# Kernel tuning notes

Hardware: AMD Instinct MI355X
Metric: run time of the kernel (lower is better)

Reference implementation:

```python
import jax, jax.numpy as jnp
import numpy as np

DIM = 512
N_HEADS = 8
N_LAYERS = 2
N_BLOCKS = 9 * N_LAYERS
B = 8
L_LEN = V_LEN = A_LEN = 512
L_DIM, V_DIM, A_DIM = 768, 640, 205
N_CLASSES = 9


def setup_inputs() -> dict:
    key = jax.random.key(0)
    ks = jax.random.split(key, 16)
    s = 0.02
    return {
        'l': jax.random.normal(ks[0], (B, L_LEN, L_DIM), jnp.float32),
        'v': jax.random.normal(ks[1], (B, V_LEN, V_DIM), jnp.float32),
        'a': jax.random.normal(ks[2], (B, A_LEN, A_DIM), jnp.float32),
        'l_mask': jnp.ones((B, L_LEN), jnp.float32),
        'v_mask': jnp.ones((B, V_LEN), jnp.float32),
        'a_mask': jnp.ones((B, A_LEN), jnp.float32),
        'wl': jax.random.normal(ks[3], (L_DIM, DIM), jnp.float32) * s,
        'wv': jax.random.normal(ks[4], (V_DIM, DIM), jnp.float32) * s,
        'wa': jax.random.normal(ks[5], (A_DIM, DIM), jnp.float32) * s,
        'n1_g': jnp.ones((DIM,), jnp.float32),
        'n1_b': jnp.zeros((DIM,), jnp.float32),
        'proj_w': jax.random.normal(ks[6], (N_BLOCKS, DIM, DIM), jnp.float32) * s,
        'minus_w': jax.random.normal(ks[7], (N_BLOCKS, 2 * DIM, DIM), jnp.float32) * s,
        'n2_g': jnp.ones((N_BLOCKS, DIM), jnp.float32),
        'n2_b': jnp.zeros((N_BLOCKS, DIM), jnp.float32),
        'c': jnp.full((N_BLOCKS,), 0.1, jnp.float32),
        'clf_w': jax.random.normal(ks[8], (6 * N_LAYERS * DIM, N_CLASSES), jnp.float32) * s,
    }


def _ln(x, g, b, eps=1e-5):
    mu = jnp.mean(x, axis=-1, keepdims=True)
    var = jnp.mean((x - mu) ** 2, axis=-1, keepdims=True)
    return (x - mu) * jax.lax.rsqrt(var + eps) * g + b


def reference(l, v, a, l_mask, v_mask, a_mask, wl, wv, wa, n1_g, n1_b,
              proj_w, minus_w, n2_g, n2_b, c, clf_w):
    hd = DIM // N_HEADS
    inv_sqrt = 1.0 / np.sqrt(hd).astype(np.float32)

    def block(i, q_in, kv, mask, scores_prev):
        Bq, Lq, D = q_in.shape
        qh = q_in.reshape(Bq, Lq, N_HEADS, hd)
        kh = kv.reshape(Bq, kv.shape[1], N_HEADS, hd)  # k and v are the same raw tensor
        scores = jnp.einsum('bqhd,bkhd->bhqk', qh, kh) * inv_sqrt
        if scores_prev is not None:
            scores = scores + c[i] * scores_prev
        scores = scores - 1e8 * (1.0 - mask[:, None, None, :])
        att = jax.nn.softmax(scores, axis=-1)
        ctx = jnp.einsum('bhqk,bkhd->bqhd', att, kh).reshape(Bq, Lq, D)
        x = ctx @ proj_w[i]  # proj, no bias; dropout is identity (eval)
        out = _ln(jnp.concatenate([q_in, x], axis=-1) @ minus_w[i], n2_g[i], n2_b[i])
        return out, scores

    def stream(q0, kv, mask, off, outs):
        q, s = q0, None
        for j in range(N_LAYERS):
            q, s = block(off * N_LAYERS + j, q, kv, mask, s)
            outs.append(q)

    # Unify_Dimension
    lu = _ln(l @ wl, n1_g, n1_b)
    vu = _ln(v @ wv, n1_g, n1_b)
    au = _ln(a @ wa, n1_g, n1_b)

    l_list, v_list, a_list = [], [], []
    stream(lu, lu, l_mask, 0, l_list)
    stream(lu, vu, v_mask, 1, l_list)
    stream(lu, au, a_mask, 2, l_list)
    stream(vu, vu, v_mask, 3, v_list)
    stream(vu, lu, l_mask, 4, v_list)
    stream(vu, au, a_mask, 5, v_list)
    stream(au, au, a_mask, 6, a_list)
    stream(au, lu, l_mask, 7, a_list)
    stream(au, vu, v_mask, 8, a_list)

    lc = jnp.concatenate(l_list, axis=2)  # [B, l_len, 3*n_layers*dim]
    vc = jnp.concatenate(v_list, axis=2)
    ac = jnp.concatenate(a_list, axis=2)
    x = jnp.concatenate([lc, ac, vc], axis=1)  # note order: l, a, v (as in source)
    feats = jnp.concatenate([jnp.mean(x, axis=1), jnp.max(x, axis=1)], axis=1)
    return feats @ clf_w
```

## Files before the change

### kernel.cpp

```cpp
#include <hip/hip_runtime.h>
#include <cstdint>
#include <cstddef>

#define DEV __device__ __forceinline__

typedef __attribute__((ext_vector_type(8))) short short8;
typedef __attribute__((ext_vector_type(4))) float floatx4;
typedef unsigned short u16;
typedef unsigned int u32;

union Frag { short8 s8; uint4 u4; uint2 u2[2]; u16 us[8]; };

DEV float b2f(u16 u) { union { float f; u32 i; } v; v.i = ((u32)u) << 16; return v.f; }
DEV u16 f2b(float f) {
  union { float f; u32 i; } v; v.f = f; u32 x = v.i;
  return (u16)((x + 0x7fffu + ((x >> 16) & 1u)) >> 16);
}
DEV floatx4 mfma16(short8 a, short8 b, floatx4 c) {
  return __builtin_amdgcn_mfma_f32_16x16x32_bf16(a, b, c, 0, 0, 0);
}
DEV void gl_lds16(const u16* g, u16* l) {
  __builtin_amdgcn_global_load_lds(
      (const __attribute__((address_space(1))) void*)g,
      (__attribute__((address_space(3))) void*)l, 16, 0, 0);
}

__global__ void det_kernel(const u32* __restrict__ mask, int* __restrict__ flag)
{
  if (threadIdx.x == 0 && blockIdx.x == 0)
    *flag = (mask[0] == 0x3F803F80u) ? 0 : 1;
}

struct ConvArgs {
  const void* src[17];
  u16* dst[17];
  int n[17];
  int bstart[17];
};

__global__ __launch_bounds__(256, 4)
void convert_all_kernel(ConvArgs a, const int* __restrict__ flag)
{
  const int bid = blockIdx.x;
  int seg = 0;
  #pragma unroll
  for (int i = 1; i < 17; i++) if (bid >= a.bstart[i]) seg = i;
  const int n = a.n[seg];
  const int base = (bid - a.bstart[seg]) * 1024 + threadIdx.x * 4;
  if (base >= n) return;
  const int f32mode = *flag;
  if (base + 4 <= n) {
    union { uint2 v; u16 u[4]; } o;
    if (f32mode) {
      const float* s = (const float*)a.src[seg] + base;
      float4 f = *(const float4*)s;
      o.u[0] = f2b(f.x); o.u[1] = f2b(f.y); o.u[2] = f2b(f.z); o.u[3] = f2b(f.w);
    } else {
      o.v = *(const uint2*)((const u16*)a.src[seg] + base);
    }
    *(uint2*)(a.dst[seg] + base) = o.v;
  } else {
    for (int k = base; k < n; k++) {
      if (f32mode) a.dst[seg][k] = f2b(((const float*)a.src[seg])[k]);
      else         a.dst[seg][k] = ((const u16*)a.src[seg])[k];
    }
  }
}

__global__ __launch_bounds__(256, 2)
void transpose_kernel(const u16* __restrict__ S, u16* __restrict__ D,
                      int R, int dstStride, int srcZ, int dstZ)
{
  __shared__ u16 tile[64 * 72];
  const u16* src = S + (size_t)blockIdx.z * srcZ;
  u16* dst = D + (size_t)blockIdx.z * dstZ;
  const int r0 = blockIdx.x * 64, c0 = blockIdx.y * 64;
  const int t = threadIdx.x;
  const int row = t >> 2, cc = (t & 3) * 16;
  if (r0 + 64 <= R) {
    uint4 v0 = *(const uint4*)(src + (size_t)(r0 + row) * 512 + c0 + cc);
    uint4 v1 = *(const uint4*)(src + (size_t)(r0 + row) * 512 + c0 + cc + 8);
    *(uint4*)&tile[row * 72 + cc] = v0;
    *(uint4*)&tile[row * 72 + cc + 8] = v1;
  } else {
    bool ok = (r0 + row) < R;
    for (int j = 0; j < 16; j++)
      tile[row * 72 + cc + j] = ok ? src[(size_t)(r0 + row) * 512 + c0 + cc + j] : (u16)0;
  }
  __syncthreads();
  const int cl = t >> 2, rc = (t & 3) * 16;
  if (r0 + 64 <= dstStride) {
    union { uint4 v[2]; u16 u[16]; } o;
    #pragma unroll
    for (int j = 0; j < 16; j++) o.u[j] = tile[(rc + j) * 72 + cl];
    u16* gd = dst + (size_t)(c0 + cl) * dstStride + r0 + rc;
    *(uint4*)gd = o.v[0];
    *(uint4*)(gd + 8) = o.v[1];
  } else {
    for (int j = 0; j < 16; j++) {
      int rr = r0 + rc + j;
      if (rr < dstStride) dst[(size_t)(c0 + cl) * dstStride + rr] = tile[(rc + j) * 72 + cl];
    }
  }
}

__global__ __launch_bounds__(256, 4)
void gemm_kernel(const u16* __restrict__ A1, int lda1, int az1,
                 const u16* __restrict__ A2, int lda2, int az2,
                 const u16* __restrict__ B1, int ldb1, int bz1,
                 const u16* __restrict__ B2, int ldb2, int bz2,
                 u16* __restrict__ O, int oz,
                 int Ktot, int Ksplit, int KAvalid, int flags)
{
  __shared__ u16 gbuf[18432];
  u16* As = gbuf;
  u16* Bs = gbuf + 4096;

  const int z = blockIdx.z;
  const int m0 = blockIdx.x * 128, n0 = blockIdx.y * 128;
  const int t = threadIdx.x, w = t >> 6, l = t & 63, l15 = l & 15, quad = l >> 4;
  const int zA = (flags & 4) ? (z / 3) : z;
  const u16* A1p = A1 + (size_t)zA * az1;
  const u16* A2p = A2 ? (A2 + (size_t)z * az2) : nullptr;
  const u16* B1p = B1 + (size_t)z * bz1;
  const u16* B2p = B2 ? (B2 + (size_t)z * bz2) : nullptr;
  u16* Op = O + (size_t)z * oz;

  const int c0r = t >> 2;
  const int c0k = t & 3;
  u16* AsW = As + (size_t)t * 8;
  u16* BsW = Bs + (size_t)t * 8;

  floatx4 acc[4][4];
  #pragma unroll
  for (int i = 0; i < 4; i++)
    #pragma unroll
    for (int j = 0; j < 4; j++) {
      acc[i][j][0] = 0.f; acc[i][j][1] = 0.f; acc[i][j][2] = 0.f; acc[i][j][3] = 0.f;
    }

  const int nsteps = Ktot >> 5;
  const int mb = (w & 1) * 64, nb = (w >> 1) * 64;
  for (int ks = 0; ks < nsteps; ks++) {
    const int k0 = ks * 32;
    const bool s2 = (k0 >= Ksplit);
    const u16* Ab = s2 ? A2p : A1p;
    const int la = s2 ? lda2 : lda1;
    const u16* Bb = s2 ? B2p : B1p;
    const int lb = s2 ? ldb2 : ldb1;
    const int kl = k0 - (s2 ? Ksplit : 0);
    const u16* ga0 = Ab + (size_t)(m0 + c0r) * la + kl + c0k * 8;
    const u16* ga1 = Ab + (size_t)(m0 + c0r + 64) * la + kl + c0k * 8;
    const u16* gb0 = Bb + (size_t)(n0 + c0r) * lb + kl + c0k * 8;
    const u16* gb1 = Bb + (size_t)(n0 + c0r + 64) * lb + kl + c0k * 8;

    __syncthreads();
    gl_lds16(gb0, BsW);
    gl_lds16(gb1, BsW + 2048);
    if (!(flags & 1)) {
      gl_lds16(ga0, AsW);
      gl_lds16(ga1, AsW + 2048);
    } else {
      union { uint4 v; u16 u[8]; } tA[2];
      #pragma unroll
      for (int i = 0; i < 2; i++) {
        const u16* gp = i ? ga1 : ga0;
        for (int j = 0; j < 8; j++) {
          int k = kl + c0k * 8 + j;
          tA[i].u[j] = (k < KAvalid) ? gp[j] : (u16)0;
        }
      }
      *(uint4*)AsW = tA[0].v;
      *(uint4*)(AsW + 2048) = tA[1].v;
    }
    __syncthreads();

    Frag fa[4], fb[4];
    #pragma unroll
    for (int i = 0; i < 4; i++) {
      fa[i].u4 = *(const uint4*)&As[(mb + i * 16 + l15) * 32 + quad * 8];
      fb[i].u4 = *(const uint4*)&Bs[(nb + i * 16 + l15) * 32 + quad * 8];
    }
    #pragma unroll
    for (int i = 0; i < 4; i++)
      #pragma unroll
      for (int j = 0; j < 4; j++)
        acc[i][j] = mfma16(fa[i].s8, fb[j].s8, acc[i][j]);
  }

  __syncthreads();
  u16* strip = gbuf + w * 4608;
  if (!(flags & 2)) {
    #pragma unroll
    for (int i = 0; i < 4; i++)
      #pragma unroll
      for (int j = 0; j < 4; j++)
        #pragma unroll
        for (int rr = 0; rr < 4; rr++)
          strip[(i * 16 + quad * 4 + rr) * 72 + j * 16 + l15] = f2b(acc[i][j][rr]);
    const int row = l >> 3, cc = l & 7;
    #pragma unroll
    for (int i = 0; i < 8; i++) {
      uint4 v = *(const uint4*)&strip[(i * 8 + row) * 72 + cc * 8];
      *(uint4*)(Op + (size_t)(m0 + mb + i * 8 + row) * 512 + n0 + nb + cc * 8) = v;
    }
  } else {
    #pragma unroll
    for (int i = 0; i < 4; i++)
      #pragma unroll
      for (int j = 0; j < 4; j++)
        #pragma unroll
        for (int rr = 0; rr < 4; rr++)
          strip[(j * 16 + l15) * 72 + i * 16 + quad * 4 + rr] = f2b(acc[i][j][rr]);
    const int row = l >> 3, cc = l & 7;
    #pragma unroll
    for (int i = 0; i < 8; i++) {
      uint4 v = *(const uint4*)&strip[(i * 8 + row) * 72 + cc * 8];
      *(uint4*)(Op + (size_t)(n0 + nb + i * 8 + row) * 512 + m0 + mb + cc * 8) = v;
    }
  }
}

__global__ __launch_bounds__(256, 2)
void ln_kernel(const u16* __restrict__ In, u16* __restrict__ Out,
               const u16* __restrict__ G, const u16* __restrict__ Bb,
               int inz, int outz, int gz)
{
  const int z = blockIdx.y;
  const u16* in = In + (size_t)z * inz;
  u16* out = Out + (size_t)z * outz;
  const u16* g = G + (size_t)z * gz;
  const u16* bb = Bb + (size_t)z * gz;
  const int t = threadIdx.x, w = t >> 6, l = t & 63;
  const int row = blockIdx.x * 4 + w;
  union { uint4 v; u16 u[8]; } xv, gv, bv, ov;
  xv.v = *(const uint4*)(in + (size_t)row * 512 + l * 8);
  float x[8]; float s1 = 0.f, s2 = 0.f;
  #pragma unroll
  for (int j = 0; j < 8; j++) { x[j] = b2f(xv.u[j]); s1 += x[j]; s2 += x[j] * x[j]; }
  #pragma unroll
  for (int m = 1; m < 64; m <<= 1) { s1 += __shfl_xor(s1, m); s2 += __shfl_xor(s2, m); }
  float mu = s1 * (1.0f / 512.0f);
  float var = s2 * (1.0f / 512.0f) - mu * mu;
  float rs = rsqrtf(var + 1e-5f);
  gv.v = *(const uint4*)(g + l * 8);
  bv.v = *(const uint4*)(bb + l * 8);
  #pragma unroll
  for (int j = 0; j < 8; j++) ov.u[j] = f2b((x[j] - mu) * rs * b2f(gv.u[j]) + b2f(bv.u[j]));
  *(uint4*)(out + (size_t)row * 512 + l * 8) = ov.v;
}

__global__ __launch_bounds__(256, 2)
void flash_kernel(const u16* __restrict__ U, const u16* __restrict__ OUT,
                  u16* __restrict__ CTX,
                  const u16* __restrict__ mask_l, const u16* __restrict__ mask_v,
                  const u16* __restrict__ mask_a, const u16* __restrict__ cvec,
                  int layer)
{
  __shared__ u16 sm[26624];
  u16* madd = sm + 26112;
  const int QS = 0, PO = 8704, KS = 17408, KT = 21760;

  const int bx = blockIdx.x;
  const int qblk = bx & 3;
  const int rest = bx >> 2;
  const int h = rest & 7, b = (rest >> 3) & 7, s = rest >> 6;
  const int t = threadIdx.x, w = t >> 6, l = t & 63, l15 = l & 15, quad = l >> 4;

  const int qm = s / 3;
  const int kvmodt[9] = {0, 1, 2, 1, 0, 2, 2, 0, 1};
  const int km = kvmodt[s];
  const size_t SZ = (size_t)4096 * 512;

  const u16* qptr; const u16* q0ptr = nullptr; float cv = 0.f;
  if (layer == 0) {
    qptr = U + (size_t)qm * SZ;
  } else {
    qptr = OUT + (size_t)(2 * s) * SZ;
    q0ptr = U + (size_t)qm * SZ;
    cv = b2f(cvec[2 * s + 1]);
  }
  const u16* kptr = U + (size_t)km * SZ;
  const u16* mptr = (km == 0) ? mask_l : ((km == 1) ? mask_v : mask_a);
  const float msc = 1.0f + cv;

  for (int i = t; i < 512; i += 256)
    madd[i] = f2b(-1e8f * (1.0f - b2f(mptr[b * 512 + i])) * msc);

  const size_t gqbase = (size_t)b * 512 * 512 + (size_t)(qblk * 128) * 512 + h * 64;
  const size_t gkbase = (size_t)b * 512 * 512 + h * 64;

  for (int i = 0; i < 4; i++) {
    int c = i * 256 + t, q = c >> 3, dc = c & 7;
    union { uint4 v; u16 u[8]; uint2 h2[2]; } raw, o;
    raw.v = *(const uint4*)(qptr + gqbase + (size_t)q * 512 + dc * 8);
    if (q0ptr) {
      union { uint4 v; u16 u[8]; } raw0;
      raw0.v = *(const uint4*)(q0ptr + gqbase + (size_t)q * 512 + dc * 8);
      #pragma unroll
      for (int j = 0; j < 8; j++) o.u[j] = f2b((b2f(raw.u[j]) + cv * b2f(raw0.u[j])) * 0.125f);
    } else {
      #pragma unroll
      for (int j = 0; j < 8; j++) o.u[j] = f2b(b2f(raw.u[j]) * 0.125f);
    }
    u16* dst = sm + QS + q * 68 + dc * 8;
    *(uint2*)dst = o.h2[0];
    *(uint2*)(dst + 4) = o.h2[1];
  }
  __syncthreads();

  float m_run[2], l_run[2];
  floatx4 acc[4][2];
  #pragma unroll
  for (int i = 0; i < 2; i++) {
    m_run[i] = -1e30f; l_run[i] = 0.f;
    #pragma unroll
    for (int d = 0; d < 4; d++) { acc[d][i][0] = 0.f; acc[d][i][1] = 0.f; acc[d][i][2] = 0.f; acc[d][i][3] = 0.f; }
  }

  for (int slab = 0; slab < 8; slab++) {
    for (int i = 0; i < 2; i++) {
      int c = i * 256 + t, kk = c >> 3, dc = c & 7;
      union { uint4 v; u16 u[8]; uint2 h2[2]; } raw;
      raw.v = *(const uint4*)(kptr + gkbase + (size_t)(slab * 64 + kk) * 512 + dc * 8);
      u16* ksd = sm + KS + kk * 68 + dc * 8;
      *(uint2*)ksd = raw.h2[0];
      *(uint2*)(ksd + 4) = raw.h2[1];
      #pragma unroll
      for (int j = 0; j < 8; j++) sm[KT + (dc * 8 + j) * 68 + kk] = raw.u[j];
    }
    __syncthreads();

    Frag afr[4][2], bfr[2][2];
    #pragma unroll
    for (int kt = 0; kt < 4; kt++)
      #pragma unroll
      for (int st = 0; st < 2; st++) {
        const u16* p = sm + KS + (kt * 16 + l15) * 68 + st * 32 + quad * 8;
        afr[kt][st].u2[0] = *(const uint2*)p;
        afr[kt][st].u2[1] = *(const uint2*)(p + 4);
      }
    #pragma unroll
    for (int qt = 0; qt < 2; qt++)
      #pragma unroll
      for (int st = 0; st < 2; st++) {
        const u16* p = sm + QS + (w * 32 + qt * 16 + l15) * 68 + st * 32 + quad * 8;
        bfr[qt][st].u2[0] = *(const uint2*)p;
        bfr[qt][st].u2[1] = *(const uint2*)(p + 4);
      }
    floatx4 S[2][4];
    #pragma unroll
    for (int qt = 0; qt < 2; qt++)
      #pragma unroll
      for (int kt = 0; kt < 4; kt++) {
        floatx4 zz = {0.f, 0.f, 0.f, 0.f};
        zz = mfma16(afr[kt][0].s8, bfr[qt][0].s8, zz);
        zz = mfma16(afr[kt][1].s8, bfr[qt][1].s8, zz);
        S[qt][kt] = zz;
      }
    float mdv[4][4];
    #pragma unroll
    for (int kt = 0; kt < 4; kt++)
      #pragma unroll
      for (int rr = 0; rr < 4; rr++) mdv[kt][rr] = b2f(madd[slab * 64 + kt * 16 + quad * 4 + rr]);

    #pragma unroll
    for (int qt = 0; qt < 2; qt++) {
      float mx = -1e30f;
      #pragma unroll
      for (int kt = 0; kt < 4; kt++)
        #pragma unroll
        for (int rr = 0; rr < 4; rr++) {
          S[qt][kt][rr] += mdv[kt][rr];
          mx = fmaxf(mx, S[qt][kt][rr]);
        }
      mx = fmaxf(mx, __shfl_xor(mx, 16));
      mx = fmaxf(mx, __shfl_xor(mx, 32));
      float mnew = fmaxf(m_run[qt], mx);
      float alpha = __expf(m_run[qt] - mnew);
      m_run[qt] = mnew;
      #pragma unroll
      for (int dt = 0; dt < 4; dt++)
        #pragma unroll
        for (int rr = 0; rr < 4; rr++) acc[dt][qt][rr] *= alpha;
      float ps = 0.f;
      #pragma unroll
      for (int kt = 0; kt < 4; kt++) {
        union { uint2 v; u16 u[4]; } pk;
        #pragma unroll
        for (int rr = 0; rr < 4; rr++) {
          float p = __expf(S[qt][kt][rr] - mnew);
          ps += p;
          pk.u[rr] = f2b(p);
        }
        *(uint2*)(sm + PO + (w * 32 + qt * 16 + l15) * 68 + kt * 16 + quad * 4) = pk.v;
      }
      ps += __shfl_xor(ps, 16);
      ps += __shfl_xor(ps, 32);
      l_run[qt] = l_run[qt] * alpha + ps;
    }

    Frag kfr[4][2], pfr[2][2];
    #pragma unroll
    for (int dt = 0; dt < 4; dt++)
      #pragma unroll
      for (int k2 = 0; k2 < 2; k2++) {
        const u16* p = sm + KT + (dt * 16 + l15) * 68 + k2 * 32 + quad * 8;
        kfr[dt][k2].u2[0] = *(const uint2*)p;
        kfr[dt][k2].u2[1] = *(const uint2*)(p + 4);
      }
    #pragma unroll
    for (int qt = 0; qt < 2; qt++)
      #pragma unroll
      for (int k2 = 0; k2 < 2; k2++) {
        const u16* p = sm + PO + (w * 32 + qt * 16 + l15) * 68 + k2 * 32 + quad * 8;
        pfr[qt][k2].u2[0] = *(const uint2*)p;
        pfr[qt][k2].u2[1] = *(const uint2*)(p + 4);
      }
    #pragma unroll
    for (int dt = 0; dt < 4; dt++)
      #pragma unroll
      for (int qt = 0; qt < 2; qt++) {
        acc[dt][qt] = mfma16(kfr[dt][0].s8, pfr[qt][0].s8, acc[dt][qt]);
        acc[dt][qt] = mfma16(kfr[dt][1].s8, pfr[qt][1].s8, acc[dt][qt]);
      }
    __syncthreads();
  }

  u16* strip = sm + KS + w * 2176;
  const size_t cbase = (size_t)s * SZ + (size_t)b * 512 * 512 + h * 64;
  #pragma unroll
  for (int qt = 0; qt < 2; qt++) {
    float rs = 1.0f / l_run[qt];
    #pragma unroll
    for (int dt = 0; dt < 4; dt++) {
      union { uint2 v; u16 u[4]; } pk;
      #pragma unroll
      for (int rr = 0; rr < 4; rr++) pk.u[rr] = f2b(acc[dt][qt][rr] * rs);
      *(uint2*)(strip + l15 * 68 + dt * 16 + quad * 4) = pk.v;
    }
    const int row = l >> 2, cc = l & 3;
    const u16* sp = strip + row * 68 + cc * 16;
    uint4 v0 = *(const uint4*)sp;
    uint4 v1 = *(const uint4*)(sp + 8);
    int q = qblk * 128 + w * 32 + qt * 16 + row;
    u16* gd = CTX + cbase + (size_t)q * 512 + cc * 16;
    *(uint4*)gd = v0;
    *(uint4*)(gd + 8) = v1;
  }
}

__global__ __launch_bounds__(256, 2)
void feats_kernel(const u16* __restrict__ OUT, float* __restrict__ F)
{
  const int b = blockIdx.y, t = threadIdx.x;
  const int jl = t & 63, qp = t >> 6;
  const int j = blockIdx.x * 64 + jl;
  const int e = j >> 9, col = j & 511, sub = e >> 1, lay = e & 1;
  const int g0[3] = {0, 6, 3};
  float sum = 0.f, mx = -3e38f;
  for (int gi = 0; gi < 3; gi++) {
    int sid = g0[gi] + sub;
    const u16* base = OUT + ((size_t)(sid * 2 + lay) * 4096 + b * 512 + qp * 128) * 512 + col;
    #pragma unroll 8
    for (int q = 0; q < 128; q++) {
      float v = b2f(base[(size_t)q * 512]);
      sum += v;
      mx = fmaxf(mx, v);
    }
  }
  __shared__ float rsm[256], rmm[256];
  rsm[t] = sum; rmm[t] = mx;
  __syncthreads();
  if (qp == 0) {
    float ts = rsm[jl] + rsm[64 + jl] + rsm[128 + jl] + rsm[192 + jl];
    float tm = fmaxf(fmaxf(rmm[jl], rmm[64 + jl]), fmaxf(rmm[128 + jl], rmm[192 + jl]));
    F[(size_t)b * 6144 + j] = ts * (1.0f / 1536.0f);
    F[(size_t)b * 6144 + 3072 + j] = tm;
  }
}

__global__ __launch_bounds__(256, 2)
void clf_kernel(const float* __restrict__ F, const u16* __restrict__ Wc,
                void* __restrict__ OutD, const int* __restrict__ flag)
{
  const int b = blockIdx.x, t = threadIdx.x;
  float pa[9];
  #pragma unroll
  for (int c = 0; c < 9; c++) pa[c] = 0.f;
  for (int j = t; j < 6144; j += 256) {
    float f = F[(size_t)b * 6144 + j];
    #pragma unroll
    for (int c = 0; c < 9; c++) pa[c] += f * b2f(Wc[(size_t)j * 9 + c]);
  }
  __shared__ float red[9 * 256];
  #pragma unroll
  for (int c = 0; c < 9; c++) red[c * 256 + t] = pa[c];
  __syncthreads();
  for (int sft = 128; sft > 0; sft >>= 1) {
    if (t < sft) {
      #pragma unroll
      for (int c = 0; c < 9; c++) red[c * 256 + t] += red[c * 256 + t + sft];
    }
    __syncthreads();
  }
  if (t < 9) {
    if (*flag) ((float*)OutD)[b * 9 + t] = red[t * 256];
    else       ((u16*)OutD)[b * 9 + t] = f2b(red[t * 256]);
  }
}

extern "C" void kernel_launch(void* const* d_in, const int* in_sizes, int n_in,
                              void* d_out, int out_size, void* d_ws, size_t ws_size,
                              hipStream_t stream)
{
  (void)n_in; (void)out_size; (void)ws_size;
  const size_t SZ = (size_t)4096 * 512;

  u16* Wp  = (u16*)d_ws;
  u16* U   = Wp;
  u16* Y   = U + 3 * SZ;
  u16* CTX = Y + 9 * SZ;
  u16* OUTb = CTX + 9 * SZ;
  u16* BtM = OUTb + 18 * SZ;
  u16* W2t = BtM + (size_t)18 * 512 * 1024;
  u16* wlT = W2t + (size_t)18 * 512 * 512;
  u16* wvT = wlT + (size_t)512 * 768;
  u16* waT = wvT + (size_t)512 * 640;
  u16* sm0 = waT + (size_t)512 * 224;
  float* F = (float*)sm0;  sm0 += (size_t)2 * 8 * 6144;
  int* flag = (int*)sm0;   sm0 += 2;
  u16* cml  = sm0; sm0 += 4096;
  u16* cmv  = sm0; sm0 += 4096;
  u16* cma  = sm0; sm0 += 4096;
  u16* cn1g = sm0; sm0 += 512;
  u16* cn1b = sm0; sm0 += 512;
  u16* cn2g = sm0; sm0 += 9216;
  u16* cn2b = sm0; sm0 += 9216;
  u16* ccv  = sm0; sm0 += 32;
  u16* ccw  = sm0; sm0 += 55296;
  u16* cl  = CTX;
  u16* cv2 = CTX + 3145728;
  u16* ca  = CTX + 5767168;
  u16* cmw = OUTb;
  u16* cpw = OUTb + 9437184;
  u16* cwl = OUTb + 14155776;
  u16* cwv = cwl + 393216;
  u16* cwa = cwv + 327680;

  det_kernel<<<1, 64, 0, stream>>>((const u32*)d_in[3], flag);

  ConvArgs ca_args;
  u16* cdst[17] = {cl, cv2, ca, cml, cmv, cma, cwl, cwv, cwa, cn1g, cn1b,
                   cpw, cmw, cn2g, cn2b, ccv, ccw};
  int btot = 0;
  for (int i = 0; i < 17; i++) {
    ca_args.src[i] = d_in[i];
    ca_args.dst[i] = cdst[i];
    ca_args.n[i] = in_sizes[i];
    ca_args.bstart[i] = btot;
    btot += (in_sizes[i] + 1023) / 1024;
  }
  convert_all_kernel<<<btot, 256, 0, stream>>>(ca_args, flag);

  transpose_kernel<<<dim3(12, 8, 1), 256, 0, stream>>>(cwl, wlT, 768, 768, 0, 0);
  transpose_kernel<<<dim3(10, 8, 1), 256, 0, stream>>>(cwv, wvT, 640, 640, 0, 0);
  transpose_kernel<<<dim3(4, 8, 1), 256, 0, stream>>>(cwa, waT, 205, 224, 0, 0);
  transpose_kernel<<<dim3(16, 8, 18), 256, 0, stream>>>(cmw, BtM, 1024, 1024, 1024 * 512, 512 * 1024);

  gemm_kernel<<<dim3(32, 4, 1), 256, 0, stream>>>(
      cl, 768, 0, nullptr, 0, 0, wlT, 768, 0, nullptr, 0, 0,
      Y, 0, 768, 768, 768, 0);
  gemm_kernel<<<dim3(32, 4, 1), 256, 0, stream>>>(
      cv2, 640, 0, nullptr, 0, 0, wvT, 640, 0, nullptr, 0, 0,
      Y + SZ, 0, 640, 640, 640, 0);
  gemm_kernel<<<dim3(32, 4, 1), 256, 0, stream>>>(
      ca, 205, 0, nullptr, 0, 0, waT, 224, 0, nullptr, 0, 0,
      Y + 2 * SZ, 0, 224, 224, 205, 1);
  ln_kernel<<<dim3(1024, 3), 256, 0, stream>>>(Y, U, cn1g, cn1b, (int)SZ, (int)SZ, 0);

  gemm_kernel<<<dim3(4, 4, 18), 256, 0, stream>>>(
      cpw, 512, 512 * 512, nullptr, 0, 0,
      BtM + 512, 1024, 512 * 1024, nullptr, 0, 0,
      W2t, 512 * 512, 512, 512, 512, 2);

  for (int layer = 0; layer < 2; layer++) {
    flash_kernel<<<2304, 256, 0, stream>>>(U, OUTb, CTX, cml, cmv, cma, ccv, layer);
    const u16* A1 = layer ? OUTb : U;
    int az1 = layer ? (int)(2 * SZ) : (int)SZ;
    int fl = layer ? 0 : 4;
    gemm_kernel<<<dim3(32, 4, 9), 256, 0, stream>>>(
        A1, 512, az1, CTX, 512, (int)SZ,
        BtM + (size_t)layer * 512 * 1024, 1024, 2 * 512 * 1024,
        W2t + (size_t)layer * 512 * 512, 512, 2 * 512 * 512,
        Y, (int)SZ, 1024, 512, 1024, fl);
    ln_kernel<<<dim3(1024, 9), 256, 0, stream>>>(
        Y, OUTb + (size_t)layer * SZ, cn2g + layer * 512, cn2b + layer * 512,
        (int)SZ, (int)(2 * SZ), 1024);
  }

  feats_kernel<<<dim3(48, 8), 256, 0, stream>>>(OUTb, F);
  clf_kernel<<<8, 256, 0, stream>>>(F, ccw, d_out, flag);
}
```

Measured before the change: 602.0 us.

## Drop online-softmax max tracking, use pre-transposed K and fold mask into MFMA init

Adds transpose kernels that build a transposed copy of each unified modality in a spare scratch region of the output buffer. The flash kernel then loads the K^T tile with vector loads instead of scalar LDS scatter stores. Scores are pre-scaled by log2e so exp2f can be used, and the mask bias goes into the MFMA accumulator init. The running max and rescaling are removed, and Q fragments are hoisted out of the slab loop; block index order is also changed. Without max subtraction, overflow is possible if scores grow large, so correctness depends on the score range that LayerNormed inputs produce.

```diff
diff --git a/kernel.cpp b/kernel.cpp
--- a/kernel.cpp
+++ b/kernel.cpp
@@ -251,8 +251,8 @@
 }
 
 __global__ __launch_bounds__(256, 2)
-void flash_kernel(const u16* __restrict__ U, const u16* __restrict__ OUT,
-                  u16* __restrict__ CTX,
+void flash_kernel(const u16* __restrict__ U, const u16* __restrict__ Ut,
+                  const u16* __restrict__ OUT, u16* __restrict__ CTX,
                   const u16* __restrict__ mask_l, const u16* __restrict__ mask_v,
                   const u16* __restrict__ mask_a, const u16* __restrict__ cvec,
                   int layer)
@@ -262,15 +262,16 @@
   const int QS = 0, PO = 8704, KS = 17408, KT = 21760;
 
   const int bx = blockIdx.x;
-  const int qblk = bx & 3;
-  const int rest = bx >> 2;
-  const int h = rest & 7, b = (rest >> 3) & 7, s = rest >> 6;
+  const int qblk = bx / 576;
+  const int rest = bx - qblk * 576;
+  const int s = rest >> 6, b = (rest >> 3) & 7, h = rest & 7;
   const int t = threadIdx.x, w = t >> 6, l = t & 63, l15 = l & 15, quad = l >> 4;
 
   const int qm = s / 3;
   const int kvmodt[9] = {0, 1, 2, 1, 0, 2, 2, 0, 1};
   const int km = kvmodt[s];
   const size_t SZ = (size_t)4096 * 512;
+  const float LOG2E = 1.44269504f;
 
   const u16* qptr; const u16* q0ptr = nullptr; float cv = 0.f;
   if (layer == 0) {
@@ -281,11 +282,13 @@
     cv = b2f(cvec[2 * s + 1]);
   }
   const u16* kptr = U + (size_t)km * SZ;
+  const u16* ktp = Ut + (size_t)(2 * km) * SZ + (size_t)b * 262144;
   const u16* mptr = (km == 0) ? mask_l : ((km == 1) ? mask_v : mask_a);
-  const float msc = 1.0f + cv;
+  const float msc = (1.0f + cv) * (-1e8f) * LOG2E;
+  const float scl = 0.125f * LOG2E;
 
   for (int i = t; i < 512; i += 256)
-    madd[i] = f2b(-1e8f * (1.0f - b2f(mptr[b * 512 + i])) * msc);
+    madd[i] = f2b((1.0f - b2f(mptr[b * 512 + i])) * msc);
 
   const size_t gqbase = (size_t)b * 512 * 512 + (size_t)(qblk * 128) * 512 + h * 64;
   const size_t gkbase = (size_t)b * 512 * 512 + h * 64;
@@ -298,10 +301,10 @@
       union { uint4 v; u16 u[8]; } raw0;
       raw0.v = *(const uint4*)(q0ptr + gqbase + (size_t)q * 512 + dc * 8);
       #pragma unroll
-      for (int j = 0; j < 8; j++) o.u[j] = f2b((b2f(raw.u[j]) + cv * b2f(raw0.u[j])) * 0.125f);
+      for (int j = 0; j < 8; j++) o.u[j] = f2b((b2f(raw.u[j]) + cv * b2f(raw0.u[j])) * scl);
     } else {
       #pragma unroll
-      for (int j = 0; j < 8; j++) o.u[j] = f2b(b2f(raw.u[j]) * 0.125f);
+      for (int j = 0; j < 8; j++) o.u[j] = f2b(b2f(raw.u[j]) * scl);
     }
     u16* dst = sm + QS + q * 68 + dc * 8;
     *(uint2*)dst = o.h2[0];
@@ -309,29 +312,40 @@
   }
   __syncthreads();
 
-  float m_run[2], l_run[2];
+  Frag bfr[2][2];
+  #pragma unroll
+  for (int qt = 0; qt < 2; qt++)
+    #pragma unroll
+    for (int st = 0; st < 2; st++) {
+      const u16* p = sm + QS + (w * 32 + qt * 16 + l15) * 68 + st * 32 + quad * 8;
+      bfr[qt][st].u2[0] = *(const uint2*)p;
+      bfr[qt][st].u2[1] = *(const uint2*)(p + 4);
+    }
+
+  float l_run[2] = {0.f, 0.f};
   floatx4 acc[4][2];
   #pragma unroll
-  for (int i = 0; i < 2; i++) {
-    m_run[i] = -1e30f; l_run[i] = 0.f;
+  for (int i = 0; i < 2; i++)
     #pragma unroll
     for (int d = 0; d < 4; d++) { acc[d][i][0] = 0.f; acc[d][i][1] = 0.f; acc[d][i][2] = 0.f; acc[d][i][3] = 0.f; }
-  }
 
   for (int slab = 0; slab < 8; slab++) {
     for (int i = 0; i < 2; i++) {
       int c = i * 256 + t, kk = c >> 3, dc = c & 7;
-      union { uint4 v; u16 u[8]; uint2 h2[2]; } raw;
+      union { uint4 v; uint2 h2[2]; } raw;
       raw.v = *(const uint4*)(kptr + gkbase + (size_t)(slab * 64 + kk) * 512 + dc * 8);
       u16* ksd = sm + KS + kk * 68 + dc * 8;
       *(uint2*)ksd = raw.h2[0];
       *(uint2*)(ksd + 4) = raw.h2[1];
-      #pragma unroll
-      for (int j = 0; j < 8; j++) sm[KT + (dc * 8 + j) * 68 + kk] = raw.u[j];
+      union { uint4 v; uint2 h2[2]; } rawt;
+      rawt.v = *(const uint4*)(ktp + (size_t)(h * 64 + kk) * 512 + slab * 64 + dc * 8);
+      u16* ktd = sm + KT + kk * 68 + dc * 8;
+      *(uint2*)ktd = rawt.h2[0];
+      *(uint2*)(ktd + 4) = rawt.h2[1];
     }
     __syncthreads();
 
-    Frag afr[4][2], bfr[2][2];
+    Frag afr[4][2];
     #pragma unroll
     for (int kt = 0; kt < 4; kt++)
       #pragma unroll
@@ -340,56 +354,31 @@
         afr[kt][st].u2[0] = *(const uint2*)p;
         afr[kt][st].u2[1] = *(const uint2*)(p + 4);
       }
-    #pragma unroll
-    for (int qt = 0; qt < 2; qt++)
-      #pragma unroll
-      for (int st = 0; st < 2; st++) {
-        const u16* p = sm + QS + (w * 32 + qt * 16 + l15) * 68 + st * 32 + quad * 8;
-        bfr[qt][st].u2[0] = *(const uint2*)p;
-        bfr[qt][st].u2[1] = *(const uint2*)(p + 4);
-      }
-    floatx4 S[2][4];
-    #pragma unroll
-    for (int qt = 0; qt < 2; qt++)
+    floatx4 cinit[4];
+    #pragma unroll
+    for (int kt = 0; kt < 4; kt++) {
+      union { uint2 v; u16 u[4]; } mv;
+      mv.v = *(const uint2*)&madd[slab * 64 + kt * 16 + quad * 4];
+      #pragma unroll
+      for (int rr = 0; rr < 4; rr++) cinit[kt][rr] = b2f(mv.u[rr]);
+    }
+    #pragma unroll
+    for (int qt = 0; qt < 2; qt++) {
+      floatx4 S[4];
       #pragma unroll
       for (int kt = 0; kt < 4; kt++) {
-        floatx4 zz = {0.f, 0.f, 0.f, 0.f};
+        floatx4 zz = cinit[kt];
         zz = mfma16(afr[kt][0].s8, bfr[qt][0].s8, zz);
         zz = mfma16(afr[kt][1].s8, bfr[qt][1].s8, zz);
-        S[qt][kt] = zz;
-      }
-    float mdv[4][4];
-    #pragma unroll
-    for (int kt = 0; kt < 4; kt++)
-      #pragma unroll
-      for (int rr = 0; rr < 4; rr++) mdv[kt][rr] = b2f(madd[slab * 64 + kt * 16 + quad * 4 + rr]);
-
-    #pragma unroll
-    for (int qt = 0; qt < 2; qt++) {
-      float mx = -1e30f;
-      #pragma unroll
-      for (int kt = 0; kt < 4; kt++)
-        #pragma unroll
-        for (int rr = 0; rr < 4; rr++) {
-          S[qt][kt][rr] += mdv[kt][rr];
-          mx = fmaxf(mx, S[qt][kt][rr]);
-        }
-      mx = fmaxf(mx, __shfl_xor(mx, 16));
-      mx = fmaxf(mx, __shfl_xor(mx, 32));
-      float mnew = fmaxf(m_run[qt], mx);
-      float alpha = __expf(m_run[qt] - mnew);
-      m_run[qt] = mnew;
-      #pragma unroll
-      for (int dt = 0; dt < 4; dt++)
-        #pragma unroll
-        for (int rr = 0; rr < 4; rr++) acc[dt][qt][rr] *= alpha;
+        S[kt] = zz;
+      }
       float ps = 0.f;
       #pragma unroll
       for (int kt = 0; kt < 4; kt++) {
         union { uint2 v; u16 u[4]; } pk;
         #pragma unroll
         for (int rr = 0; rr < 4; rr++) {
-          float p = __expf(S[qt][kt][rr] - mnew);
+          float p = exp2f(S[kt][rr]);
           ps += p;
           pk.u[rr] = f2b(p);
         }
@@ -397,7 +386,7 @@
       }
       ps += __shfl_xor(ps, 16);
       ps += __shfl_xor(ps, 32);
-      l_run[qt] = l_run[qt] * alpha + ps;
+      l_run[qt] += ps;
     }
 
     Frag kfr[4][2], pfr[2][2];
@@ -547,6 +536,7 @@
   u16* cwl = OUTb + 14155776;
   u16* cwv = cwl + 393216;
   u16* cwa = cwv + 327680;
+  u16* Ut = OUTb + SZ;
 
   det_kernel<<<1, 64, 0, stream>>>((const u32*)d_in[3], flag);
 
@@ -568,6 +558,11 @@
   transpose_kernel<<<dim3(4, 8, 1), 256, 0, stream>>>(cwa, waT, 205, 224, 0, 0);
   transpose_kernel<<<dim3(16, 8, 18), 256, 0, stream>>>(cmw, BtM, 1024, 1024, 1024 * 512, 512 * 1024);
 
+  gemm_kernel<<<dim3(4, 4, 18), 256, 0, stream>>>(
+      cpw, 512, 512 * 512, nullptr, 0, 0,
+      BtM + 512, 1024, 512 * 1024, nullptr, 0, 0,
+      W2t, 512 * 512, 512, 512, 512, 2);
+
   gemm_kernel<<<dim3(32, 4, 1), 256, 0, stream>>>(
       cl, 768, 0, nullptr, 0, 0, wlT, 768, 0, nullptr, 0, 0,
       Y, 0, 768, 768, 768, 0);
@@ -579,13 +574,12 @@
       Y + 2 * SZ, 0, 224, 224, 205, 1);
   ln_kernel<<<dim3(1024, 3), 256, 0, stream>>>(Y, U, cn1g, cn1b, (int)SZ, (int)SZ, 0);
 
-  gemm_kernel<<<dim3(4, 4, 18), 256, 0, stream>>>(
-      cpw, 512, 512 * 512, nullptr, 0, 0,
-      BtM + 512, 1024, 512 * 1024, nullptr, 0, 0,
-      W2t, 512 * 512, 512, 512, 512, 2);
+  for (int m = 0; m < 3; m++)
+    transpose_kernel<<<dim3(8, 8, 8), 256, 0, stream>>>(
+        U + (size_t)m * SZ, Ut + (size_t)(2 * m) * SZ, 512, 512, 262144, 262144);
 
   for (int layer = 0; layer < 2; layer++) {
-    flash_kernel<<<2304, 256, 0, stream>>>(U, OUTb, CTX, cml, cmv, cma, ccv, layer);
+    flash_kernel<<<2304, 256, 0, stream>>>(U, Ut, OUTb, CTX, cml, cmv, cma, ccv, layer);
     const u16* A1 = layer ? OUTb : U;
     int az1 = layer ? (int)(2 * SZ) : (int)SZ;
     int fl = layer ? 0 : 4;
```

Measured after the change: 631.8 us. +5.0%, slower.
